# Optimization experiments

Hardware: AMD Instinct MI355X
Metric: run time of the kernel (lower is better)

The kernel has to match this reference:

```python
import jax, jax.numpy as jnp
import numpy as np

N_NODES = 50000
N_EDGES = 800000
NODE_DIM = 64
EDGE_DIM = 32
HIDDEN = 128
OUT_DIM = 32
N_LAYERS = 3
NUM_GRAPHS = 128


def setup_inputs() -> dict:
    key = jax.random.key(0)
    ks = jax.random.split(key, 20)
    s = 0.05
    inp = {
        "x": jax.random.normal(ks[0], (N_NODES, NODE_DIM), dtype=jnp.float32),
        "edge_attr": jax.random.normal(ks[1], (N_EDGES, EDGE_DIM), dtype=jnp.float32),
        "edge_index": jax.random.randint(ks[2], (2, N_EDGES), 0, N_NODES, dtype=jnp.int32),
        "batch": jnp.sort(jax.random.randint(ks[3], (N_NODES,), 0, NUM_GRAPHS, dtype=jnp.int32)),
        # per-interaction params, stacked on leading layer axis
        "W_dense": jax.random.normal(ks[4], (N_LAYERS, NODE_DIM, NODE_DIM)) * s,
        "filt_W1": jax.random.normal(ks[5], (N_LAYERS, EDGE_DIM, HIDDEN)) * s,
        "filt_b1": jnp.zeros((N_LAYERS, HIDDEN)),
        "filt_W2": jax.random.normal(ks[6], (N_LAYERS, HIDDEN, NODE_DIM)) * s,
        "filt_b2": jnp.zeros((N_LAYERS, NODE_DIM)),
        "attn_v": jax.random.normal(ks[7], (N_LAYERS, NODE_DIM)) * s,
        "out_W1": jax.random.normal(ks[8], (N_LAYERS, NODE_DIM, HIDDEN)) * s,
        "out_b1": jnp.zeros((N_LAYERS, HIDDEN)),
        "out_W2": jax.random.normal(ks[9], (N_LAYERS, HIDDEN, NODE_DIM)) * s,
        "out_b2": jnp.zeros((N_LAYERS, NODE_DIM)),
        # output network
        "net_W1": jax.random.normal(ks[10], (NODE_DIM, HIDDEN)) * s,
        "net_b1": jnp.zeros((HIDDEN,)),
        "net_W2": jax.random.normal(ks[11], (HIDDEN, OUT_DIM)) * s,
        "net_b2": jnp.zeros((OUT_DIM,)),
    }
    return inp


def _mlp2(x, W1, b1, W2, b2):
    # 2-layer MLP with tanh after first layer (matches MLP(num_layers=2, act='tanh'))
    return jnp.tanh(x @ W1 + b1) @ W2 + b2


def reference(x, edge_attr, W_dense, filt_W1, filt_b1, filt_W2, filt_b2,
              attn_v, out_W1, out_b1, out_W2, out_b2,
              net_W1, net_b1, net_W2, net_b2, edge_index, batch):
    n_nodes = x.shape[0]
    src, tgt = edge_index[0], edge_index[1]
    h = x
    for i in range(N_LAYERS):
        hd = h @ W_dense[i]                                   # initial_dense (no bias)
        edge_w = _mlp2(edge_attr, filt_W1[i], filt_b1[i], filt_W2[i], filt_b2[i])  # [E, D]
        messages = hd[src] * edge_w                           # [E, D]
        # per-target segment softmax over attention scores
        scores = messages @ attn_v[i]                         # [E]
        seg_max = jax.ops.segment_max(scores, tgt, num_segments=n_nodes)
        exp_s = jnp.exp(scores - seg_max[tgt])
        denom = jax.ops.segment_sum(exp_s, tgt, num_segments=n_nodes)
        attn_w = exp_s / denom[tgt]                           # [E]
        messages = messages * attn_w[:, None]
        agg = jax.ops.segment_sum(messages, tgt, num_segments=n_nodes)  # [N, D]
        delta = _mlp2(agg, out_W1[i], out_b1[i], out_W2[i], out_b2[i])
        h = h + delta                                         # residual
    # mean pooling per graph
    pooled = jax.ops.segment_sum(h, batch, num_segments=NUM_GRAPHS)
    counts = jnp.bincount(batch, length=NUM_GRAPHS)
    pooled = pooled / jnp.maximum(counts, 1)[:, None].astype(h.dtype)
    out = _mlp2(pooled, net_W1, net_b1, net_W2, net_b2)       # [G, OUT_DIM]
    return out
```

## Files before the change

kernel.cpp:

```cpp
#include <hip/hip_runtime.h>
#include <hip/hip_bf16.h>
#include <math.h>

#define NODE_DIM 64
#define EDGE_DIM 32
#define HIDDEN   128
#define OUT_DIM  32
#define N_LAYERS 3
#define NGRAPH   128

typedef __attribute__((ext_vector_type(8))) short bf16x8;
typedef __attribute__((ext_vector_type(4))) float f32x4;

__device__ __forceinline__ unsigned short f2bf(float f) {
    unsigned u = __float_as_uint(f);
    u = (u + 0x7fffu + ((u >> 16) & 1u)) >> 16;
    return (unsigned short)u;
}
__device__ __forceinline__ float bf2f(unsigned short h) {
    return __uint_as_float((unsigned)h << 16);
}
__device__ __forceinline__ float fast_tanh(float x) {
    float ax = fabsf(x);
    float e = __expf(-2.f * ax);
    float r = __builtin_amdgcn_rcpf(1.f + e);
    float t = (1.f - e) * r;
    return __builtin_copysignf(t, x);
}

__global__ __launch_bounds__(256) void coarse_hist_kernel(
    const int* __restrict__ tgt, int* __restrict__ Hc, int E, int C, int NB) {
    __shared__ int lh[512];
    int blk = blockIdx.x, tid = threadIdx.x;
    for (int b = tid; b < C; b += 256) lh[b] = 0;
    __syncthreads();
    int base = blk * 4096;
#pragma unroll
    for (int i = 0; i < 16; ++i) {
        int e = base + i * 256 + tid;
        if (e < E) atomicAdd(&lh[tgt[e] >> 7], 1);
    }
    __syncthreads();
    for (int b = tid; b < C; b += 256) Hc[(size_t)b * NB + blk] = lh[b];
}

__global__ __launch_bounds__(256) void scan1_kernel(const int* __restrict__ c,
                                                    int* __restrict__ o,
                                                    int* __restrict__ bsum, int n) {
    __shared__ int sh[256];
    int b = blockIdx.x, t = threadIdx.x;
    int i = b * 256 + t;
    int v = (i < n) ? c[i] : 0;
    sh[t] = v;
    __syncthreads();
    for (int d = 1; d < 256; d <<= 1) {
        int u = (t >= d) ? sh[t - d] : 0;
        __syncthreads();
        sh[t] += u;
        __syncthreads();
    }
    if (i < n) o[i] = sh[t] - v;
    if (t == 255) bsum[b] = sh[255];
}

__global__ void scan2_kernel(int* __restrict__ bsum, int nb) {
    __shared__ int sh[1024];
    int t = threadIdx.x;
    int v = (t < nb) ? bsum[t] : 0;
    sh[t] = v;
    __syncthreads();
    for (int d = 1; d < 1024; d <<= 1) {
        int u = (t >= d) ? sh[t - d] : 0;
        __syncthreads();
        sh[t] += u;
        __syncthreads();
    }
    if (t < nb) bsum[t] = sh[t] - v;
}

__global__ __launch_bounds__(256) void scan3_kernel(int* __restrict__ o,
                                                    const int* __restrict__ bsum, int n) {
    int i = blockIdx.x * 256 + threadIdx.x;
    if (i < n) o[i] += bsum[blockIdx.x];
}

__global__ __launch_bounds__(256) void coarse_scatter_kernel(
    const int* __restrict__ tgt, const int* __restrict__ Sc,
    int* __restrict__ tgtc, int* __restrict__ ec, int E, int C, int NB) {
    __shared__ int lb[512];
    int blk = blockIdx.x, tid = threadIdx.x;
    for (int b = tid; b < C; b += 256) lb[b] = Sc[(size_t)b * NB + blk];
    __syncthreads();
    int base = blk * 4096;
#pragma unroll
    for (int i = 0; i < 16; ++i) {
        int e = base + i * 256 + tid;
        if (e < E) {
            int t = tgt[e];
            int pos = atomicAdd(&lb[t >> 7], 1);
            tgtc[pos] = t;
            ec[pos] = e;
        }
    }
}

__global__ __launch_bounds__(256) void fine_sort_kernel(
    const int* __restrict__ Sc, const int* __restrict__ tgtc,
    const int* __restrict__ ec, const int* __restrict__ src,
    int* __restrict__ off, int* __restrict__ eidx, int* __restrict__ srcp,
    int E, int N, int C, int NB) {
    __shared__ int fh[128], fs[128], rb[128];
    int b = blockIdx.x, tid = threadIdx.x;
    int cb0 = Sc[(size_t)b * NB];
    int cb1 = (b + 1 < C) ? Sc[(size_t)(b + 1) * NB] : E;
    if (tid < 128) fh[tid] = 0;
    __syncthreads();
    for (int p = cb0 + tid; p < cb1; p += 256) atomicAdd(&fh[tgtc[p] & 127], 1);
    __syncthreads();
    if (tid < 128) fs[tid] = fh[tid];
    __syncthreads();
    for (int d = 1; d < 128; d <<= 1) {
        int v = 0;
        if (tid < 128 && tid >= d) v = fs[tid - d];
        __syncthreads();
        if (tid < 128) fs[tid] += v;
        __syncthreads();
    }
    if (tid < 128) {
        int ex = fs[tid] - fh[tid];
        rb[tid] = ex;
        int node = (b << 7) + tid;
        if (node < N) off[node] = cb0 + ex;
    }
    if (b == C - 1 && tid == 0) off[N] = E;
    __syncthreads();
    for (int p = cb0 + tid; p < cb1; p += 256) {
        int t = tgtc[p];
        int r = atomicAdd(&rb[t & 127], 1);
        int fpos = cb0 + r;
        int e = ec[p];
        eidx[fpos] = e;
        srcp[fpos] = src[e];
    }
}

__global__ void gbound_kernel(const int* __restrict__ batch, int* __restrict__ goff,
                              int N, int G) {
    int i = blockIdx.x * 256 + threadIdx.x;
    if (i >= N) return;
    int b = batch[i];
    if (i == 0) {
        for (int g = 0; g <= b; ++g) goff[g] = 0;
    } else {
        int bp = batch[i - 1];
        for (int g = bp + 1; g <= b; ++g) goff[g] = i;
    }
    if (i == N - 1) {
        for (int g = b + 1; g <= G; ++g) goff[g] = N;
    }
}

__global__ __launch_bounds__(256) void perm_ea_kernel(
    const float* __restrict__ ea, const int* __restrict__ eidx,
    unsigned short* __restrict__ out, int E) {
    int p = blockIdx.x * 256 + threadIdx.x;
    if (p >= E) return;
    int e = eidx[p];
    const float4* r = (const float4*)(ea + (size_t)e * EDGE_DIM);
    union { unsigned short us[EDGE_DIM]; uint4 u4[EDGE_DIM / 8]; } tmp;
#pragma unroll
    for (int q = 0; q < EDGE_DIM / 4; ++q) {
        float4 v = r[q];
        tmp.us[4 * q]     = f2bf(v.x);
        tmp.us[4 * q + 1] = f2bf(v.y);
        tmp.us[4 * q + 2] = f2bf(v.z);
        tmp.us[4 * q + 3] = f2bf(v.w);
    }
    uint4* o = (uint4*)(out + (size_t)p * EDGE_DIM);
#pragma unroll
    for (int k = 0; k < EDGE_DIM / 8; ++k) o[k] = tmp.u4[k];
}

__global__ void swizzle_w_kernel(const float* __restrict__ fW1, const float* __restrict__ fW2,
                                 const float* __restrict__ oW1, const float* __restrict__ oW2,
                                 unsigned short* __restrict__ W1sw, unsigned short* __restrict__ W2sw,
                                 unsigned short* __restrict__ oW1sw, unsigned short* __restrict__ oW2sw) {
    int i = blockIdx.x / 56, r = blockIdx.x % 56;
    int L = threadIdx.x;
    int e = L & 15, q = L >> 4;
    const float* W;
    unsigned short* out;
    int K, M, t;
    if (r < 8)       { W = fW1 + (size_t)i * EDGE_DIM * HIDDEN;  out = W1sw  + (size_t)i * 8 * 512;  K = EDGE_DIM; M = HIDDEN;   t = r; }
    else if (r < 24) { W = fW2 + (size_t)i * HIDDEN * NODE_DIM;  out = W2sw  + (size_t)i * 16 * 512; K = HIDDEN;   M = NODE_DIM; t = r - 8; }
    else if (r < 40) { W = oW1 + (size_t)i * NODE_DIM * HIDDEN;  out = oW1sw + (size_t)i * 16 * 512; K = NODE_DIM; M = HIDDEN;   t = r - 24; }
    else             { W = oW2 + (size_t)i * HIDDEN * NODE_DIM;  out = oW2sw + (size_t)i * 16 * 512; K = HIDDEN;   M = NODE_DIM; t = r - 40; }
    int nc = K >> 5;
    int mt = t / nc, s = t - mt * nc;
    union { unsigned short us[8]; uint4 u4; } pk;
#pragma unroll
    for (int j = 0; j < 8; ++j)
        pk.us[j] = f2bf(W[(size_t)(32 * s + 8 * q + j) * M + 16 * mt + e]);
    *(uint4*)(out + ((size_t)t * 64 + L) * 8) = pk.u4;
}

#define HSTRIDE 136

__global__ __launch_bounds__(256) void edge_mfma_kernel(
    const unsigned short* __restrict__ ea_p, const float* __restrict__ hd,
    const unsigned short* __restrict__ W1sw, const float* __restrict__ b1,
    const unsigned short* __restrict__ W2sw, const float* __restrict__ b2,
    const float* __restrict__ av, const int* __restrict__ srcp,
    unsigned short* __restrict__ msg, float* __restrict__ score, int E) {
    __shared__ unsigned short Hl[4][16 * HSTRIDE];
    int wave = threadIdx.x >> 6, lane = threadIdx.x & 63;
    int e = lane & 15, q = lane >> 4;
    int p0 = blockIdx.x * 64 + wave * 16;
    if (p0 >= E) return;

    bf16x8 eaf = *(const bf16x8*)(ea_p + (size_t)(p0 + e) * EDGE_DIM + q * 8);

    f32x4 c1[8];
#pragma unroll
    for (int t = 0; t < 8; ++t) {
        bf16x8 a = *(const bf16x8*)(W1sw + (t * 64 + lane) * 8);
        c1[t] = __builtin_amdgcn_mfma_f32_16x16x32_bf16(a, eaf, (f32x4){0.f, 0.f, 0.f, 0.f}, 0, 0, 0);
    }

    unsigned short* hrow = &Hl[wave][e * HSTRIDE];
#pragma unroll
    for (int t = 0; t < 8; ++t) {
        float4 b = *(const float4*)(b1 + 16 * t + 4 * q);
        unsigned h0 = f2bf(fast_tanh(c1[t][0] + b.x));
        unsigned h1 = f2bf(fast_tanh(c1[t][1] + b.y));
        unsigned h2 = f2bf(fast_tanh(c1[t][2] + b.z));
        unsigned h3 = f2bf(fast_tanh(c1[t][3] + b.w));
        uint2 pk;
        pk.x = h0 | (h1 << 16);
        pk.y = h2 | (h3 << 16);
        *(uint2*)(hrow + 16 * t + 4 * q) = pk;
    }

    f32x4 c2[4] = {{0.f, 0.f, 0.f, 0.f}, {0.f, 0.f, 0.f, 0.f},
                   {0.f, 0.f, 0.f, 0.f}, {0.f, 0.f, 0.f, 0.f}};
#pragma unroll
    for (int s = 0; s < 4; ++s) {
        bf16x8 hf = *(const bf16x8*)(hrow + 32 * s + 8 * q);
#pragma unroll
        for (int nt = 0; nt < 4; ++nt) {
            bf16x8 a = *(const bf16x8*)(W2sw + ((nt * 4 + s) * 64 + lane) * 8);
            c2[nt] = __builtin_amdgcn_mfma_f32_16x16x32_bf16(a, hf, c2[nt], 0, 0, 0);
        }
    }

    int sidx = srcp[p0 + e];
    float sc = 0.f;
#pragma unroll
    for (int nt = 0; nt < 4; ++nt) {
        float4 bb = *(const float4*)(b2 + 16 * nt + 4 * q);
        float4 vv = *(const float4*)(av + 16 * nt + 4 * q);
        float4 hh = *(const float4*)(hd + (size_t)sidx * NODE_DIM + 16 * nt + 4 * q);
        float m0 = (c2[nt][0] + bb.x) * hh.x;
        float m1 = (c2[nt][1] + bb.y) * hh.y;
        float m2 = (c2[nt][2] + bb.z) * hh.z;
        float m3 = (c2[nt][3] + bb.w) * hh.w;
        uint2 pk;
        pk.x = (unsigned)f2bf(m0) | ((unsigned)f2bf(m1) << 16);
        pk.y = (unsigned)f2bf(m2) | ((unsigned)f2bf(m3) << 16);
        *(uint2*)(msg + (size_t)(p0 + e) * NODE_DIM + 16 * nt + 4 * q) = pk;
        sc += m0 * vv.x + m1 * vv.y + m2 * vv.z + m3 * vv.w;
    }
    sc += __shfl_xor(sc, 16, 64);
    sc += __shfl_xor(sc, 32, 64);
    if (q == 0) score[p0 + e] = sc;
}

__global__ __launch_bounds__(256) void node_mlp_kernel(
    const float* __restrict__ agg,
    const unsigned short* __restrict__ W1sw, const float* __restrict__ b1,
    const unsigned short* __restrict__ W2sw, const float* __restrict__ b2,
    float* __restrict__ h, int N) {
    __shared__ unsigned short Hl[4][16 * HSTRIDE];
    int wave = threadIdx.x >> 6, lane = threadIdx.x & 63;
    int e = lane & 15, q = lane >> 4;
    int n0 = (blockIdx.x * 4 + wave) * 16;
    if (n0 >= N) return;
    int ne = n0 + e;
    int neC = ne < N ? ne : N - 1;
    bool ok = ne < N;

    bf16x8 bfr[2];
#pragma unroll
    for (int s = 0; s < 2; ++s) {
        const float4* ar = (const float4*)(agg + (size_t)neC * NODE_DIM + 32 * s + 8 * q);
        float4 x0 = ar[0], x1 = ar[1];
        union { bf16x8 v; unsigned short us[8]; } u;
        u.us[0] = f2bf(x0.x); u.us[1] = f2bf(x0.y);
        u.us[2] = f2bf(x0.z); u.us[3] = f2bf(x0.w);
        u.us[4] = f2bf(x1.x); u.us[5] = f2bf(x1.y);
        u.us[6] = f2bf(x1.z); u.us[7] = f2bf(x1.w);
        bfr[s] = u.v;
    }

    f32x4 c1[8];
#pragma unroll
    for (int t = 0; t < 8; ++t) {
        bf16x8 a0 = *(const bf16x8*)(W1sw + ((t * 2 + 0) * 64 + lane) * 8);
        bf16x8 a1 = *(const bf16x8*)(W1sw + ((t * 2 + 1) * 64 + lane) * 8);
        c1[t] = __builtin_amdgcn_mfma_f32_16x16x32_bf16(a0, bfr[0], (f32x4){0.f, 0.f, 0.f, 0.f}, 0, 0, 0);
        c1[t] = __builtin_amdgcn_mfma_f32_16x16x32_bf16(a1, bfr[1], c1[t], 0, 0, 0);
    }

    unsigned short* hrow = &Hl[wave][e * HSTRIDE];
#pragma unroll
    for (int t = 0; t < 8; ++t) {
        float4 b = *(const float4*)(b1 + 16 * t + 4 * q);
        unsigned h0 = f2bf(fast_tanh(c1[t][0] + b.x));
        unsigned h1 = f2bf(fast_tanh(c1[t][1] + b.y));
        unsigned h2 = f2bf(fast_tanh(c1[t][2] + b.z));
        unsigned h3 = f2bf(fast_tanh(c1[t][3] + b.w));
        uint2 pk;
        pk.x = h0 | (h1 << 16);
        pk.y = h2 | (h3 << 16);
        *(uint2*)(hrow + 16 * t + 4 * q) = pk;
    }

    f32x4 c2[4] = {{0.f, 0.f, 0.f, 0.f}, {0.f, 0.f, 0.f, 0.f},
                   {0.f, 0.f, 0.f, 0.f}, {0.f, 0.f, 0.f, 0.f}};
#pragma unroll
    for (int s = 0; s < 4; ++s) {
        bf16x8 hf = *(const bf16x8*)(hrow + 32 * s + 8 * q);
#pragma unroll
        for (int nt = 0; nt < 4; ++nt) {
            bf16x8 a = *(const bf16x8*)(W2sw + ((nt * 4 + s) * 64 + lane) * 8);
            c2[nt] = __builtin_amdgcn_mfma_f32_16x16x32_bf16(a, hf, c2[nt], 0, 0, 0);
        }
    }

    if (ok) {
#pragma unroll
        for (int nt = 0; nt < 4; ++nt) {
            float4 bb = *(const float4*)(b2 + 16 * nt + 4 * q);
            float4* hp = (float4*)(h + (size_t)ne * NODE_DIM + 16 * nt + 4 * q);
            float4 hv = *hp;
            hv.x += c2[nt][0] + bb.x;
            hv.y += c2[nt][1] + bb.y;
            hv.z += c2[nt][2] + bb.z;
            hv.w += c2[nt][3] + bb.w;
            *hp = hv;
        }
    }
}

template <int K, int M, bool ACT, bool RESID>
__global__ __launch_bounds__(256) void dense_kernel(
    const float* __restrict__ X, const float* __restrict__ W,
    const float* __restrict__ bias, float* __restrict__ Y, int rows) {
    int tid = blockIdx.x * 256 + threadIdx.x;
    int row = tid / M;
    int d = tid - row * M;
    if (row >= rows) return;
    if (M >= 64) row = __builtin_amdgcn_readfirstlane(row);
    const float* __restrict__ x = X + (size_t)row * K;
    float acc = bias ? bias[d] : 0.f;
#pragma unroll
    for (int k = 0; k < K; ++k) acc += x[k] * W[k * M + d];
    if (ACT) acc = fast_tanh(acc);
    if (RESID) acc += Y[(size_t)row * M + d];
    Y[(size_t)row * M + d] = acc;
}

__global__ __launch_bounds__(256) void agg_kernel(
    const unsigned short* __restrict__ msg, const float* __restrict__ score,
    const int* __restrict__ off, float* __restrict__ agg, int n) {
    int tid = blockIdx.x * 256 + threadIdx.x;
    int wid = tid >> 6;
    int lane = threadIdx.x & 63;
    if (wid >= n) return;
    wid = __builtin_amdgcn_readfirstlane(wid);
    int o0 = off[wid], o1 = off[wid + 1];
    int g = lane >> 3, s = lane & 7;
    if (o1 <= o0) {
        if (g == 0) {
            float4 z = {0.f, 0.f, 0.f, 0.f};
            float4* dst = (float4*)(agg + (size_t)wid * NODE_DIM + s * 8);
            dst[0] = z; dst[1] = z;
        }
        return;
    }
    float den = 0.f;
    float acc[8] = {0.f, 0.f, 0.f, 0.f, 0.f, 0.f, 0.f, 0.f};
    for (int p = o0; p < o1; p += 8) {
        int pe = p + g;
        int pc = (pe < o1) ? pe : (o1 - 1);
        float w = (pe < o1) ? __expf(fminf(score[pc], 60.f)) : 0.f;
        den += w;
        union { bf16x8 v; unsigned short us[8]; } eu;
        eu.v = *(const bf16x8*)(msg + (size_t)pc * NODE_DIM + s * 8);
        acc[0] += w * bf2f(eu.us[0]);
        acc[1] += w * bf2f(eu.us[1]);
        acc[2] += w * bf2f(eu.us[2]);
        acc[3] += w * bf2f(eu.us[3]);
        acc[4] += w * bf2f(eu.us[4]);
        acc[5] += w * bf2f(eu.us[5]);
        acc[6] += w * bf2f(eu.us[6]);
        acc[7] += w * bf2f(eu.us[7]);
    }
#pragma unroll
    for (int j = 0; j < 8; ++j) {
        acc[j] += __shfl_xor(acc[j], 8, 64);
        acc[j] += __shfl_xor(acc[j], 16, 64);
        acc[j] += __shfl_xor(acc[j], 32, 64);
    }
    den += __shfl_xor(den, 8, 64);
    den += __shfl_xor(den, 16, 64);
    den += __shfl_xor(den, 32, 64);
    if (g == 0) {
        float inv = __builtin_amdgcn_rcpf(den);
        inv = inv * (2.f - den * inv);
        float4 r0 = {acc[0] * inv, acc[1] * inv, acc[2] * inv, acc[3] * inv};
        float4 r1 = {acc[4] * inv, acc[5] * inv, acc[6] * inv, acc[7] * inv};
        float4* dst = (float4*)(agg + (size_t)wid * NODE_DIM + s * 8);
        dst[0] = r0; dst[1] = r1;
    }
}

__global__ __launch_bounds__(256) void pool_kernel(const float* __restrict__ h,
                                                   const int* __restrict__ goff,
                                                   float* __restrict__ pooled) {
    __shared__ float sh[4][NODE_DIM];
    int g = blockIdx.x;
    int w = threadIdx.x >> 6, d = threadIdx.x & 63;
    int o0 = goff[g], o1 = goff[g + 1];
    float acc = 0.f;
    for (int n = o0 + w; n < o1; n += 4) acc += h[(size_t)n * NODE_DIM + d];
    sh[w][d] = acc;
    __syncthreads();
    if (w == 0) {
        float sum = sh[0][d] + sh[1][d] + sh[2][d] + sh[3][d];
        int c = o1 - o0;
        if (c < 1) c = 1;
        pooled[g * NODE_DIM + d] = sum / (float)c;
    }
}

extern "C" void kernel_launch(void* const* d_in, const int* in_sizes, int n_in,
                              void* d_out, int out_size, void* d_ws, size_t ws_size,
                              hipStream_t stream) {
    const float* x         = (const float*)d_in[0];
    const float* edge_attr = (const float*)d_in[1];
    const int*   ei        = (const int*)d_in[2];
    const int*   batch     = (const int*)d_in[3];
    const float* Wd        = (const float*)d_in[4];
    const float* fW1       = (const float*)d_in[5];
    const float* fb1       = (const float*)d_in[6];
    const float* fW2       = (const float*)d_in[7];
    const float* fb2       = (const float*)d_in[8];
    const float* av        = (const float*)d_in[9];
    const float* oW1       = (const float*)d_in[10];
    const float* ob1       = (const float*)d_in[11];
    const float* oW2       = (const float*)d_in[12];
    const float* ob2       = (const float*)d_in[13];
    const float* nW1       = (const float*)d_in[14];
    const float* nb1       = (const float*)d_in[15];
    const float* nW2       = (const float*)d_in[16];
    const float* nb2       = (const float*)d_in[17];
    float* out = (float*)d_out;

    const int N = in_sizes[0] / NODE_DIM;
    const int E = in_sizes[2] / 2;
    const int G = NGRAPH;
    const int NB = (E + 4095) / 4096;
    const int C  = (N + 127) >> 7;
    const int SN = C * NB;
    const int SB = (SN + 255) / 256;

    char* base = (char*)d_ws;
    size_t pos = 0;
    auto alloc = [&](size_t bytes) -> void* {
        pos = (pos + 255) & ~(size_t)255;
        void* r = base + pos;
        pos += bytes;
        return r;
    };
    int* Hc   = (int*)alloc((size_t)SN * 4);
    int* Sc   = (int*)alloc(((size_t)SN + 1) * 4);
    int* bsum = (int*)alloc((size_t)1024 * 4);
    int* tgtc = (int*)alloc((size_t)E * 4);
    int* ec   = (int*)alloc((size_t)E * 4);
    int* off  = (int*)alloc((size_t)(N + 1) * 4);
    int* goff = (int*)alloc((size_t)(G + 1) * 4);
    int* eidx = (int*)alloc((size_t)E * 4);
    int* srcp = (int*)alloc((size_t)E * 4);
    float* score = (float*)alloc((size_t)E * 4);
    float* hd    = (float*)alloc((size_t)N * NODE_DIM * 4);
    float* h     = (float*)alloc((size_t)N * NODE_DIM * 4);
    float* agg   = (float*)alloc((size_t)N * NODE_DIM * 4);
    float* pooled = (float*)alloc((size_t)G * NODE_DIM * 4);
    float* t2     = (float*)alloc((size_t)G * HIDDEN * 4);
    unsigned short* ea_p  = (unsigned short*)alloc((size_t)E * EDGE_DIM * 2);
    unsigned short* msg   = (unsigned short*)alloc((size_t)E * NODE_DIM * 2);
    unsigned short* W1sw  = (unsigned short*)alloc((size_t)N_LAYERS * 8 * 512 * 2);
    unsigned short* W2sw  = (unsigned short*)alloc((size_t)N_LAYERS * 16 * 512 * 2);
    unsigned short* oW1sw = (unsigned short*)alloc((size_t)N_LAYERS * 16 * 512 * 2);
    unsigned short* oW2sw = (unsigned short*)alloc((size_t)N_LAYERS * 16 * 512 * 2);
    (void)ws_size;

    const int* src = ei;
    const int* tgt = ei + E;

    coarse_hist_kernel<<<NB, 256, 0, stream>>>(tgt, Hc, E, C, NB);
    scan1_kernel<<<SB, 256, 0, stream>>>(Hc, Sc, bsum, SN);
    scan2_kernel<<<1, 1024, 0, stream>>>(bsum, SB);
    scan3_kernel<<<SB, 256, 0, stream>>>(Sc, bsum, SN);
    coarse_scatter_kernel<<<NB, 256, 0, stream>>>(tgt, Sc, tgtc, ec, E, C, NB);
    fine_sort_kernel<<<C, 256, 0, stream>>>(Sc, tgtc, ec, src, off, eidx, srcp, E, N, C, NB);
    gbound_kernel<<<(N + 255) / 256, 256, 0, stream>>>(batch, goff, N, G);
    perm_ea_kernel<<<(E + 255) / 256, 256, 0, stream>>>(edge_attr, eidx, ea_p, E);
    swizzle_w_kernel<<<N_LAYERS * 56, 64, 0, stream>>>(fW1, fW2, oW1, oW2, W1sw, W2sw, oW1sw, oW2sw);
    hipMemcpyAsync(h, x, (size_t)N * NODE_DIM * 4, hipMemcpyDeviceToDevice, stream);

    const int node_tiles = (N + 15) / 16;
    for (int i = 0; i < N_LAYERS; ++i) {
        dense_kernel<NODE_DIM, NODE_DIM, false, false>
            <<<(N * NODE_DIM + 255) / 256, 256, 0, stream>>>(
                h, Wd + (size_t)i * NODE_DIM * NODE_DIM, nullptr, hd, N);
        edge_mfma_kernel<<<(E + 63) / 64, 256, 0, stream>>>(
            ea_p, hd,
            W1sw + (size_t)i * 8 * 512, fb1 + (size_t)i * HIDDEN,
            W2sw + (size_t)i * 16 * 512, fb2 + (size_t)i * NODE_DIM,
            av + (size_t)i * NODE_DIM, srcp, msg, score, E);
        agg_kernel<<<(N + 3) / 4, 256, 0, stream>>>(msg, score, off, agg, N);
        node_mlp_kernel<<<(node_tiles + 3) / 4, 256, 0, stream>>>(
            agg,
            oW1sw + (size_t)i * 16 * 512, ob1 + (size_t)i * HIDDEN,
            oW2sw + (size_t)i * 16 * 512, ob2 + (size_t)i * NODE_DIM,
            h, N);
    }

    pool_kernel<<<G, 256, 0, stream>>>(h, goff, pooled);
    dense_kernel<NODE_DIM, HIDDEN, true, false>
        <<<(G * HIDDEN + 255) / 256, 256, 0, stream>>>(pooled, nW1, nb1, t2, G);
    dense_kernel<HIDDEN, OUT_DIM, false, false>
        <<<(G * OUT_DIM + 255) / 256, 256, 0, stream>>>(t2, nW2, nb2, out, G);
}
```

Baseline: 781.7 us.

## Process two edge tiles per wave in edge kernel and simplify tanh

Each wave in the edge filter kernel now handles 32 edges as two 16-edge groups instead of one. Loads for both groups (edge attributes, source indices) are issued up front, and the per-group MLP is split into halves to lower live accumulator registers, with launch_bounds set to a minimum of 5 blocks for occupancy. The tanh helper is rewritten as 2/(1+exp(-2x))-1, which drops the abs and copysign but can overflow the exponent for large negative inputs. The grid is halved to match, and bounds checks are added for the tail.

```diff
diff --git a/kernel.cpp b/kernel.cpp
--- a/kernel.cpp
+++ b/kernel.cpp
@@ -21,11 +21,9 @@
     return __uint_as_float((unsigned)h << 16);
 }
 __device__ __forceinline__ float fast_tanh(float x) {
-    float ax = fabsf(x);
-    float e = __expf(-2.f * ax);
+    float e = __expf(-2.f * x);
     float r = __builtin_amdgcn_rcpf(1.f + e);
-    float t = (1.f - e) * r;
-    return __builtin_copysignf(t, x);
+    return __builtin_fmaf(2.f, r, -1.f);
 }
 
 __global__ __launch_bounds__(256) void coarse_hist_kernel(
@@ -206,7 +204,76 @@
 
 #define HSTRIDE 136
 
-__global__ __launch_bounds__(256) void edge_mfma_kernel(
+__device__ __forceinline__ void eg_process(
+    bf16x8 eaf, int sidx, int pdst, bool valid,
+    unsigned short* hrow, int lane, int q,
+    const unsigned short* __restrict__ W1sw, const float* __restrict__ b1,
+    const unsigned short* __restrict__ W2sw, const float* __restrict__ b2,
+    const float* __restrict__ av, const float* __restrict__ hd,
+    unsigned short* __restrict__ msg, float* __restrict__ score) {
+#pragma unroll
+    for (int th = 0; th < 2; ++th) {
+        f32x4 c[4];
+#pragma unroll
+        for (int t = 0; t < 4; ++t) {
+            bf16x8 a = *(const bf16x8*)(W1sw + ((th * 4 + t) * 64 + lane) * 8);
+            c[t] = __builtin_amdgcn_mfma_f32_16x16x32_bf16(a, eaf, (f32x4){0.f, 0.f, 0.f, 0.f}, 0, 0, 0);
+        }
+#pragma unroll
+        for (int t = 0; t < 4; ++t) {
+            int tt = th * 4 + t;
+            float4 b = *(const float4*)(b1 + 16 * tt + 4 * q);
+            unsigned h0 = f2bf(fast_tanh(c[t][0] + b.x));
+            unsigned h1 = f2bf(fast_tanh(c[t][1] + b.y));
+            unsigned h2 = f2bf(fast_tanh(c[t][2] + b.z));
+            unsigned h3 = f2bf(fast_tanh(c[t][3] + b.w));
+            uint2 pk;
+            pk.x = h0 | (h1 << 16);
+            pk.y = h2 | (h3 << 16);
+            *(uint2*)(hrow + 16 * tt + 4 * q) = pk;
+        }
+    }
+
+    float4 hv[4];
+#pragma unroll
+    for (int nt = 0; nt < 4; ++nt)
+        hv[nt] = *(const float4*)(hd + (size_t)sidx * NODE_DIM + 16 * nt + 4 * q);
+
+    float sc = 0.f;
+#pragma unroll
+    for (int np = 0; np < 2; ++np) {
+        f32x4 c2[2] = {{0.f, 0.f, 0.f, 0.f}, {0.f, 0.f, 0.f, 0.f}};
+#pragma unroll
+        for (int s = 0; s < 4; ++s) {
+            bf16x8 hf = *(const bf16x8*)(hrow + 32 * s + 8 * q);
+            bf16x8 a0 = *(const bf16x8*)(W2sw + (((2 * np + 0) * 4 + s) * 64 + lane) * 8);
+            bf16x8 a1 = *(const bf16x8*)(W2sw + (((2 * np + 1) * 4 + s) * 64 + lane) * 8);
+            c2[0] = __builtin_amdgcn_mfma_f32_16x16x32_bf16(a0, hf, c2[0], 0, 0, 0);
+            c2[1] = __builtin_amdgcn_mfma_f32_16x16x32_bf16(a1, hf, c2[1], 0, 0, 0);
+        }
+#pragma unroll
+        for (int k = 0; k < 2; ++k) {
+            int nt = 2 * np + k;
+            float4 bb = *(const float4*)(b2 + 16 * nt + 4 * q);
+            float4 vv = *(const float4*)(av + 16 * nt + 4 * q);
+            float4 hh = hv[nt];
+            float m0 = (c2[k][0] + bb.x) * hh.x;
+            float m1 = (c2[k][1] + bb.y) * hh.y;
+            float m2 = (c2[k][2] + bb.z) * hh.z;
+            float m3 = (c2[k][3] + bb.w) * hh.w;
+            uint2 pk;
+            pk.x = (unsigned)f2bf(m0) | ((unsigned)f2bf(m1) << 16);
+            pk.y = (unsigned)f2bf(m2) | ((unsigned)f2bf(m3) << 16);
+            if (valid) *(uint2*)(msg + (size_t)pdst * NODE_DIM + 16 * nt + 4 * q) = pk;
+            sc += m0 * vv.x + m1 * vv.y + m2 * vv.z + m3 * vv.w;
+        }
+    }
+    sc += __shfl_xor(sc, 16, 64);
+    sc += __shfl_xor(sc, 32, 64);
+    if (q == 0 && valid) score[pdst] = sc;
+}
+
+__global__ __launch_bounds__(256, 5) void edge_mfma_kernel(
     const unsigned short* __restrict__ ea_p, const float* __restrict__ hd,
     const unsigned short* __restrict__ W1sw, const float* __restrict__ b1,
     const unsigned short* __restrict__ W2sw, const float* __restrict__ b2,
@@ -215,64 +282,21 @@
     __shared__ unsigned short Hl[4][16 * HSTRIDE];
     int wave = threadIdx.x >> 6, lane = threadIdx.x & 63;
     int e = lane & 15, q = lane >> 4;
-    int p0 = blockIdx.x * 64 + wave * 16;
+    int p0 = blockIdx.x * 128 + wave * 32;
     if (p0 >= E) return;
-
-    bf16x8 eaf = *(const bf16x8*)(ea_p + (size_t)(p0 + e) * EDGE_DIM + q * 8);
-
-    f32x4 c1[8];
-#pragma unroll
-    for (int t = 0; t < 8; ++t) {
-        bf16x8 a = *(const bf16x8*)(W1sw + (t * 64 + lane) * 8);
-        c1[t] = __builtin_amdgcn_mfma_f32_16x16x32_bf16(a, eaf, (f32x4){0.f, 0.f, 0.f, 0.f}, 0, 0, 0);
-    }
-
+    int pA = p0 + e, pB = p0 + 16 + e;
+    int pAc = pA < E ? pA : E - 1;
+    int pBc = pB < E ? pB : E - 1;
+    bool vA = pA < E, vB = pB < E;
+
+    bf16x8 eafA = *(const bf16x8*)(ea_p + (size_t)pAc * EDGE_DIM + q * 8);
+    bf16x8 eafB = *(const bf16x8*)(ea_p + (size_t)pBc * EDGE_DIM + q * 8);
+    int sA = srcp[pAc];
+    int sB = srcp[pBc];
     unsigned short* hrow = &Hl[wave][e * HSTRIDE];
-#pragma unroll
-    for (int t = 0; t < 8; ++t) {
-        float4 b = *(const float4*)(b1 + 16 * t + 4 * q);
-        unsigned h0 = f2bf(fast_tanh(c1[t][0] + b.x));
-        unsigned h1 = f2bf(fast_tanh(c1[t][1] + b.y));
-        unsigned h2 = f2bf(fast_tanh(c1[t][2] + b.z));
-        unsigned h3 = f2bf(fast_tanh(c1[t][3] + b.w));
-        uint2 pk;
-        pk.x = h0 | (h1 << 16);
-        pk.y = h2 | (h3 << 16);
-        *(uint2*)(hrow + 16 * t + 4 * q) = pk;
-    }
-
-    f32x4 c2[4] = {{0.f, 0.f, 0.f, 0.f}, {0.f, 0.f, 0.f, 0.f},
-                   {0.f, 0.f, 0.f, 0.f}, {0.f, 0.f, 0.f, 0.f}};
-#pragma unroll
-    for (int s = 0; s < 4; ++s) {
-        bf16x8 hf = *(const bf16x8*)(hrow + 32 * s + 8 * q);
-#pragma unroll
-        for (int nt = 0; nt < 4; ++nt) {
-            bf16x8 a = *(const bf16x8*)(W2sw + ((nt * 4 + s) * 64 + lane) * 8);
-            c2[nt] = __builtin_amdgcn_mfma_f32_16x16x32_bf16(a, hf, c2[nt], 0, 0, 0);
-        }
-    }
-
-    int sidx = srcp[p0 + e];
-    float sc = 0.f;
-#pragma unroll
-    for (int nt = 0; nt < 4; ++nt) {
-        float4 bb = *(const float4*)(b2 + 16 * nt + 4 * q);
-        float4 vv = *(const float4*)(av + 16 * nt + 4 * q);
-        float4 hh = *(const float4*)(hd + (size_t)sidx * NODE_DIM + 16 * nt + 4 * q);
-        float m0 = (c2[nt][0] + bb.x) * hh.x;
-        float m1 = (c2[nt][1] + bb.y) * hh.y;
-        float m2 = (c2[nt][2] + bb.z) * hh.z;
-        float m3 = (c2[nt][3] + bb.w) * hh.w;
-        uint2 pk;
-        pk.x = (unsigned)f2bf(m0) | ((unsigned)f2bf(m1) << 16);
-        pk.y = (unsigned)f2bf(m2) | ((unsigned)f2bf(m3) << 16);
-        *(uint2*)(msg + (size_t)(p0 + e) * NODE_DIM + 16 * nt + 4 * q) = pk;
-        sc += m0 * vv.x + m1 * vv.y + m2 * vv.z + m3 * vv.w;
-    }
-    sc += __shfl_xor(sc, 16, 64);
-    sc += __shfl_xor(sc, 32, 64);
-    if (q == 0) score[p0 + e] = sc;
+
+    eg_process(eafA, sA, pA, vA, hrow, lane, q, W1sw, b1, W2sw, b2, av, hd, msg, score);
+    eg_process(eafB, sB, pB, vB, hrow, lane, q, W1sw, b1, W2sw, b2, av, hd, msg, score);
 }
 
 __global__ __launch_bounds__(256) void node_mlp_kernel(
@@ -525,7 +549,7 @@
         dense_kernel<NODE_DIM, NODE_DIM, false, false>
             <<<(N * NODE_DIM + 255) / 256, 256, 0, stream>>>(
                 h, Wd + (size_t)i * NODE_DIM * NODE_DIM, nullptr, hd, N);
-        edge_mfma_kernel<<<(E + 63) / 64, 256, 0, stream>>>(
+        edge_mfma_kernel<<<(E + 127) / 128, 256, 0, stream>>>(
             ea_p, hd,
             W1sw + (size_t)i * 8 * 512, fb1 + (size_t)i * HIDDEN,
             W2sw + (size_t)i * 16 * 512, fb2 + (size_t)i * NODE_DIM,
```

Result: slower. 1.514 ms (+93.7%).
